# Kernel optimization log

Measured on AMD Instinct MI355X. Metric: run time of the kernel, lower is better.

Reference implementation:

```python
import jax, jax.numpy as jnp
import numpy as np

EPS = 1e-5

def _ln(x, g, b):
    mu = jnp.mean(x, axis=-1, keepdims=True)
    var = jnp.mean((x - mu) ** 2, axis=-1, keepdims=True)
    return (x - mu) * jax.lax.rsqrt(var + EPS) * g + b

def setup_inputs() -> dict:
    key = jax.random.key(0)
    B, V, I, H = 32, 48, 24, 768
    ks = jax.random.split(key, 10)
    s = 0.02
    return {
        'variables': jax.random.normal(ks[0], (B, V, H), jnp.float32),
        'interventions': jax.random.normal(ks[1], (B, I, H), jnp.float32),
        # variable_encoder: Linear(H,H) + LayerNorm(H)
        'W_enc': jax.random.normal(ks[2], (H, H), jnp.float32) * s,
        'b_enc': jnp.zeros((H,), jnp.float32),
        'g_enc': jnp.ones((H,), jnp.float32),
        'be_enc': jnp.zeros((H,), jnp.float32),
        # graph_generator: Linear(2H,H) + LN(H) + ReLU + Linear(H,1) + Sigmoid
        'Wg1': jax.random.normal(ks[3], (2 * H, H), jnp.float32) * s,
        'bg1': jnp.zeros((H,), jnp.float32),
        'g_g': jnp.ones((H,), jnp.float32),
        'b_g': jnp.zeros((H,), jnp.float32),
        'Wg2': jax.random.normal(ks[4], (H, 1), jnp.float32) * s,
        'bg2': jnp.zeros((1,), jnp.float32),
        # intervention_predictor: Linear(2H,H) + LN(H) + ReLU + Linear(H,H)
        'Wi1': jax.random.normal(ks[5], (2 * H, H), jnp.float32) * s,
        'bi1': jnp.zeros((H,), jnp.float32),
        'g_i': jnp.ones((H,), jnp.float32),
        'b_i': jnp.zeros((H,), jnp.float32),
        'Wi2': jax.random.normal(ks[6], (H, H), jnp.float32) * s,
        'bi2': jnp.zeros((H,), jnp.float32),
    }

def reference(variables, interventions, W_enc, b_enc, g_enc, be_enc,
              Wg1, bg1, g_g, b_g, Wg2, bg2, Wi1, bi1, g_i, b_i, Wi2, bi2):
    H = variables.shape[-1]
    V = variables.shape[1]
    # variable encoder: Linear + LayerNorm + ReLU
    enc = jax.nn.relu(_ln(variables @ W_enc + b_enc, g_enc, be_enc))  # [B,V,H]

    # graph generator over all ordered pairs (i,j): concat([enc_i, enc_j]) @ Wg1
    # split Wg1 so the concat-matmul becomes two small GEMMs + broadcast add
    hi = jnp.einsum('bvh,hk->bvk', enc, Wg1[:H])   # contribution of enc_i
    hj = jnp.einsum('bvh,hk->bvk', enc, Wg1[H:])   # contribution of enc_j
    h = jax.nn.relu(_ln(hi[:, :, None, :] + hj[:, None, :, :] + bg1, g_g, b_g))  # [B,V,V,H]
    score = jax.nn.sigmoid(jnp.squeeze(h @ Wg2, -1) + bg2[0])  # [B,V,V]
    # diagonal (i==j) is never written in the original -> stays zero
    causal_graph = score * (1.0 - jnp.eye(V, dtype=score.dtype))

    # intervention predictor: concat([intervention_i, enc_j]) -> MLP
    ha = jnp.einsum('bih,hk->bik', interventions, Wi1[:H])  # [B,I,H]
    hb = jnp.einsum('bvh,hk->bvk', enc, Wi1[H:])            # [B,V,H]
    h2 = jax.nn.relu(_ln(ha[:, :, None, :] + hb[:, None, :, :] + bi1, g_i, b_i))  # [B,I,V,H]
    effects = h2 @ Wi2 + bi2  # [B,I,V,H]

    return (effects, causal_graph, enc)
```

## Files before the change

kernel.cpp:

```cpp
#include <hip/hip_runtime.h>
#include <math.h>

#define Bp 32
#define Vp 48
#define Ip 24
#define Hp 768
#define EPS 1e-5f

#define EFFECTS_SIZE (Bp*Ip*Vp*Hp)
#define GRAPH_SIZE   (Bp*Vp*Vp)
#define ENC_SIZE     (Bp*Vp*Hp)
#define MS           (Hp*Hp)

typedef __attribute__((ext_vector_type(8))) short short8;
typedef __attribute__((ext_vector_type(4))) float floatx4;
typedef __attribute__((ext_vector_type(4))) unsigned int uintx4;

__device__ __forceinline__ unsigned short f2bf(float f) {
    unsigned int u = __float_as_uint(f);
    u += 0x7fffu + ((u >> 16) & 1u);
    return (unsigned short)(u >> 16);
}
__device__ __forceinline__ unsigned int f2bf2(float a, float b) {
    return (unsigned int)f2bf(a) | ((unsigned int)f2bf(b) << 16);
}

__global__ __launch_bounds__(256) void pack_weights(
    const float* __restrict__ W_enc, const float* __restrict__ Wg1,
    const float* __restrict__ Wi1, const float* __restrict__ Wi2,
    unsigned short* __restrict__ packed)
{
    const int bid = blockIdx.x;
    const int m = bid / 288;
    const int rem = bid - m * 288;
    const int T = rem / 6;
    const int u = rem - T * 6;
    const float* src;
    switch (m) {
        case 0: src = W_enc; break;
        case 1: src = Wg1; break;
        case 2: src = Wg1 + Hp * Hp; break;
        case 3: src = Wi1 + Hp * Hp; break;
        case 4: src = Wi1; break;
        default: src = Wi2; break;
    }
    unsigned short* dst = packed + (size_t)m * MS;
    const int lane = threadIdx.x & 63;
    const int kq = threadIdx.x >> 6;
    const int col = T * 16 + (lane & 15);
    const int krow0 = (lane >> 4) * 8;
    const int kb = kq + 4 * u;
    unsigned int w[4];
#pragma unroll
    for (int p2 = 0; p2 < 4; ++p2) {
        float f0 = src[(size_t)(kb * 32 + krow0 + 2 * p2)     * Hp + col];
        float f1 = src[(size_t)(kb * 32 + krow0 + 2 * p2 + 1) * Hp + col];
        w[p2] = f2bf2(f0, f1);
    }
    uintx4 v; v.x = w[0]; v.y = w[1]; v.z = w[2]; v.w = w[3];
    *(uintx4*)(dst + ((size_t)(T * 24 + kb) * 64 + lane) * 8) = v;
}

__global__ __launch_bounds__(256) void convert_inputs(
    const float* __restrict__ vars, const float* __restrict__ intv,
    const float* __restrict__ bg1, const float* __restrict__ bi1,
    unsigned short* __restrict__ varb, unsigned short* __restrict__ intvb,
    float* __restrict__ bias2304)
{
    const int p = blockIdx.x * 256 + threadIdx.x;
    const int VPn = ENC_SIZE / 2;
    if (p < VPn) {
        float2 f = ((const float2*)vars)[p];
        ((unsigned int*)varb)[p] = f2bf2(f.x, f.y);
    } else {
        int q = p - VPn;
        float2 f = ((const float2*)intv)[q];
        ((unsigned int*)intvb)[q] = f2bf2(f.x, f.y);
    }
    if (blockIdx.x == 0) {
        for (int t = threadIdx.x; t < 2304; t += 256)
            bias2304[t] = (t < 768) ? 0.0f : (t < 1536 ? bg1[t - 768] : bi1[t - 1536]);
    }
}

__global__ __launch_bounds__(256) void gemm48(
    const unsigned short* __restrict__ A, const unsigned short* __restrict__ Bpk,
    const float* __restrict__ bias, float* __restrict__ C, int ldc)
{
    __shared__ unsigned short Asl[3 * 24 * 64 * 8];
    const int tid = threadIdx.x, wave = tid >> 6, lane = tid & 63;
    const int m0 = blockIdx.x * 48;

#pragma unroll
    for (int uu = 0; uu < 18; ++uu) {
        const int s = tid + 256 * uu;
        const int mt = s / 1536;
        const int r2 = s - mt * 1536;
        const int kb = r2 >> 6;
        const int L  = r2 & 63;
        const int mrow = L & 15, kq = L >> 4;
        uintx4 v = *(const uintx4*)(A + (size_t)(m0 + mt * 16 + mrow) * Hp + kb * 32 + kq * 8);
        const int phys = (mt * 24 + kb) * 64 + (L ^ (kb & 7));
        *(uintx4*)(&Asl[phys * 8]) = v;
    }
    __syncthreads();

    const int mrow = lane & 15, kq = lane >> 4;
    const floatx4 z = {0.f, 0.f, 0.f, 0.f};

#pragma unroll
    for (int G = 0; G < 2; ++G) {
        const int Tg0 = blockIdx.y * 48 + wave * 12 + G * 6;
        const unsigned short* Bbase = Bpk + (size_t)Tg0 * 12288 + lane * 8;
        floatx4 acc[3][6];
#pragma unroll
        for (int mt = 0; mt < 3; ++mt)
#pragma unroll
            for (int nt = 0; nt < 6; ++nt) acc[mt][nt] = z;

        short8 bbuf[3][6], abuf[2][3];
#pragma unroll
        for (int nt = 0; nt < 6; ++nt) {
            bbuf[0][nt] = *(const short8*)(Bbase + (size_t)nt * 12288);
            bbuf[1][nt] = *(const short8*)(Bbase + (size_t)nt * 12288 + 512);
        }
#pragma unroll
        for (int mt = 0; mt < 3; ++mt)
            abuf[0][mt] = *(const short8*)(&Asl[((mt * 24) * 64 + lane) * 8]);

#pragma unroll
        for (int kb = 0; kb < 24; ++kb) {
            if (kb + 2 < 24) {
#pragma unroll
                for (int nt = 0; nt < 6; ++nt)
                    bbuf[(kb + 2) % 3][nt] =
                        *(const short8*)(Bbase + (size_t)nt * 12288 + (kb + 2) * 512);
            }
            if (kb + 1 < 24) {
#pragma unroll
                for (int mt = 0; mt < 3; ++mt)
                    abuf[(kb + 1) & 1][mt] = *(const short8*)(
                        &Asl[((mt * 24 + kb + 1) * 64 + (lane ^ ((kb + 1) & 7))) * 8]);
            }
#pragma unroll
            for (int mt = 0; mt < 3; ++mt)
#pragma unroll
                for (int nt = 0; nt < 6; ++nt)
                    acc[mt][nt] = __builtin_amdgcn_mfma_f32_16x16x32_bf16(
                        abuf[kb & 1][mt], bbuf[kb % 3][nt], acc[mt][nt], 0, 0, 0);
        }

#pragma unroll
        for (int nt = 0; nt < 6; ++nt) {
            const int colg = (Tg0 + nt) * 16 + mrow;
            const float bv = bias ? bias[colg] : 0.0f;
#pragma unroll
            for (int mt = 0; mt < 3; ++mt)
#pragma unroll
                for (int r = 0; r < 4; ++r)
                    C[(size_t)(m0 + mt * 16 + kq * 4 + r) * ldc + colg] = acc[mt][nt][r] + bv;
        }
    }
}

__global__ __launch_bounds__(256) void ln_relu(
    const float* __restrict__ pre, const float* __restrict__ g,
    const float* __restrict__ be, float* __restrict__ encf,
    unsigned short* __restrict__ encb)
{
    const int wave = threadIdx.x >> 6, lane = threadIdx.x & 63;
    const int row = blockIdx.x * 4 + wave;
    const float2* rp = (const float2*)(pre + (size_t)row * Hp);
    float2 x[6]; float s = 0.f, q = 0.f;
#pragma unroll
    for (int c = 0; c < 6; ++c) {
        x[c] = rp[lane + 64 * c];
        s += x[c].x + x[c].y;
        q += x[c].x * x[c].x + x[c].y * x[c].y;
    }
#pragma unroll
    for (int m = 1; m < 64; m <<= 1) { s += __shfl_xor(s, m, 64); q += __shfl_xor(q, m, 64); }
    const float mu = s * (1.0f / Hp);
    const float var = q * (1.0f / Hp) - mu * mu;
    const float rs = rsqrtf(var + EPS);
    float2* of = (float2*)(encf + (size_t)row * Hp);
    unsigned int* ob = (unsigned int*)(encb + (size_t)row * Hp);
#pragma unroll
    for (int c = 0; c < 6; ++c) {
        const float2 g2 = ((const float2*)g)[lane + 64 * c];
        const float2 b2 = ((const float2*)be)[lane + 64 * c];
        float y0 = fmaxf((x[c].x - mu) * rs * g2.x + b2.x, 0.f);
        float y1 = fmaxf((x[c].y - mu) * rs * g2.y + b2.y, 0.f);
        of[lane + 64 * c] = make_float2(y0, y1);
        ob[lane + 64 * c] = f2bf2(y0, y1);
    }
}

__global__ __launch_bounds__(256) void graph_kernel(
    const float* __restrict__ ws2, const float* __restrict__ gg_,
    const float* __restrict__ bb_, const float* __restrict__ Wg2,
    const float* __restrict__ bg2, float* __restrict__ out)
{
    const int wave = threadIdx.x >> 6, lane = threadIdx.x & 63;
    const int p = blockIdx.x;
    const int b = p / Vp, i = p - b * Vp;
    const float* hi_row = ws2 + (size_t)p * 2304;
    float ri[12], gg[12], bb[12], w2[12];
#pragma unroll
    for (int c = 0; c < 12; ++c) {
        const int k = lane + 64 * c;
        ri[c] = hi_row[k]; gg[c] = gg_[k]; bb[c] = bb_[k]; w2[c] = Wg2[k];
    }
    const float bg2v = bg2[0];
    const int j0 = wave * 12;
    for (int jj = 0; jj < 12; ++jj) {
        const int j = j0 + jj;
        const float* hj_row = ws2 + (size_t)(b * Vp + j) * 2304 + 768;
        float x[12], s = 0.f, q = 0.f;
#pragma unroll
        for (int c = 0; c < 12; ++c) {
            x[c] = ri[c] + hj_row[lane + 64 * c];
            s += x[c]; q += x[c] * x[c];
        }
#pragma unroll
        for (int m = 1; m < 64; m <<= 1) { s += __shfl_xor(s, m, 64); q += __shfl_xor(q, m, 64); }
        const float mu = s * (1.0f / Hp);
        const float var = q * (1.0f / Hp) - mu * mu;
        const float rs = rsqrtf(var + EPS);
        float pd = 0.f;
#pragma unroll
        for (int c = 0; c < 12; ++c) {
            float y = fmaxf((x[c] - mu) * rs * gg[c] + bb[c], 0.f);
            pd = fmaf(y, w2[c], pd);
        }
#pragma unroll
        for (int m = 1; m < 64; m <<= 1) pd += __shfl_xor(pd, m, 64);
        if (lane == 0) {
            float sc = (i == j) ? 0.0f : 1.0f / (1.0f + expf(-(pd + bg2v)));
            out[(size_t)p * Vp + j] = sc;
        }
    }
}

__global__ __launch_bounds__(256) void effects48(
    const float* __restrict__ ha, const float* __restrict__ ws2,
    const float* __restrict__ g_i, const float* __restrict__ b_i,
    const unsigned short* __restrict__ Bpk, const float* __restrict__ bi2,
    float* __restrict__ out)
{
    __shared__ unsigned short Asl[3 * 24 * 64 * 8];
    const int tid = threadIdx.x, wave = tid >> 6, lane = tid & 63;
    const int bi = blockIdx.x;
    const int b = bi / Ip;
    const int half = lane >> 5, hl = lane & 31;

    const floatx4* hap = (const floatx4*)(ha + (size_t)bi * Hp);
    const floatx4* gp = (const floatx4*)g_i;
    const floatx4* bp = (const floatx4*)b_i;
    floatx4 hav[6], gv[6], bv[6];
#pragma unroll
    for (int t = 0; t < 3; ++t) {
        hav[2*t]   = hap[2*hl + 64*t];     hav[2*t+1] = hap[2*hl + 1 + 64*t];
        gv[2*t]    = gp[2*hl + 64*t];      gv[2*t+1]  = gp[2*hl + 1 + 64*t];
        bv[2*t]    = bp[2*hl + 64*t];      bv[2*t+1]  = bp[2*hl + 1 + 64*t];
    }

#pragma unroll
    for (int p = 0; p < 6; ++p) {
        const int u = wave * 12 + 2 * p + half;
        const floatx4* hbp = (const floatx4*)(ws2 + (size_t)(b * Vp + u) * 2304 + 1536);
        floatx4 x[6]; float s = 0.f, q = 0.f;
#pragma unroll
        for (int t = 0; t < 3; ++t) {
            x[2*t]   = hav[2*t]   + hbp[2*hl + 64*t];
            x[2*t+1] = hav[2*t+1] + hbp[2*hl + 1 + 64*t];
        }
#pragma unroll
        for (int c = 0; c < 6; ++c) {
            s += x[c].x + x[c].y + x[c].z + x[c].w;
            q += x[c].x*x[c].x + x[c].y*x[c].y + x[c].z*x[c].z + x[c].w*x[c].w;
        }
#pragma unroll
        for (int m = 1; m < 32; m <<= 1) { s += __shfl_xor(s, m, 64); q += __shfl_xor(q, m, 64); }
        const float mu = s * (1.0f / Hp);
        const float var = q * (1.0f / Hp) - mu * mu;
        const float rs = rsqrtf(var + EPS);
        const int mt = u >> 4, mrow = u & 15;
#pragma unroll
        for (int t = 0; t < 3; ++t) {
            float y0 = fmaxf((x[2*t].x   - mu) * rs * gv[2*t].x   + bv[2*t].x,   0.f);
            float y1 = fmaxf((x[2*t].y   - mu) * rs * gv[2*t].y   + bv[2*t].y,   0.f);
            float y2 = fmaxf((x[2*t].z   - mu) * rs * gv[2*t].z   + bv[2*t].z,   0.f);
            float y3 = fmaxf((x[2*t].w   - mu) * rs * gv[2*t].w   + bv[2*t].w,   0.f);
            float y4 = fmaxf((x[2*t+1].x - mu) * rs * gv[2*t+1].x + bv[2*t+1].x, 0.f);
            float y5 = fmaxf((x[2*t+1].y - mu) * rs * gv[2*t+1].y + bv[2*t+1].y, 0.f);
            float y6 = fmaxf((x[2*t+1].z - mu) * rs * gv[2*t+1].z + bv[2*t+1].z, 0.f);
            float y7 = fmaxf((x[2*t+1].w - mu) * rs * gv[2*t+1].w + bv[2*t+1].w, 0.f);
            const int cpk = hl + 32 * t;
            const int kb = cpk >> 2, kq2 = cpk & 3;
            const int phys = (mt * 24 + kb) * 64 + ((kq2 * 16 + mrow) ^ (kb & 7));
            uintx4 v;
            v.x = f2bf2(y0, y1); v.y = f2bf2(y2, y3);
            v.z = f2bf2(y4, y5); v.w = f2bf2(y6, y7);
            *(uintx4*)(&Asl[phys * 8]) = v;
        }
    }
    __syncthreads();

    const int mrow = lane & 15, kq = lane >> 4;
    const floatx4 z = {0.f, 0.f, 0.f, 0.f};
#pragma unroll
    for (int G = 0; G < 2; ++G) {
        const int Tg0 = wave * 12 + G * 6;
        const unsigned short* Bbase = Bpk + (size_t)Tg0 * 12288 + lane * 8;
        floatx4 acc[3][6];
#pragma unroll
        for (int mt = 0; mt < 3; ++mt)
#pragma unroll
            for (int nt = 0; nt < 6; ++nt) acc[mt][nt] = z;

        short8 bbuf[3][6], abuf[2][3];
#pragma unroll
        for (int nt = 0; nt < 6; ++nt) {
            bbuf[0][nt] = *(const short8*)(Bbase + (size_t)nt * 12288);
            bbuf[1][nt] = *(const short8*)(Bbase + (size_t)nt * 12288 + 512);
        }
#pragma unroll
        for (int mt = 0; mt < 3; ++mt)
            abuf[0][mt] = *(const short8*)(&Asl[((mt * 24) * 64 + lane) * 8]);

#pragma unroll
        for (int kb = 0; kb < 24; ++kb) {
            if (kb + 2 < 24) {
#pragma unroll
                for (int nt = 0; nt < 6; ++nt)
                    bbuf[(kb + 2) % 3][nt] =
                        *(const short8*)(Bbase + (size_t)nt * 12288 + (kb + 2) * 512);
            }
            if (kb + 1 < 24) {
#pragma unroll
                for (int mt = 0; mt < 3; ++mt)
                    abuf[(kb + 1) & 1][mt] = *(const short8*)(
                        &Asl[((mt * 24 + kb + 1) * 64 + (lane ^ ((kb + 1) & 7))) * 8]);
            }
#pragma unroll
            for (int mt = 0; mt < 3; ++mt)
#pragma unroll
                for (int nt = 0; nt < 6; ++nt)
                    acc[mt][nt] = __builtin_amdgcn_mfma_f32_16x16x32_bf16(
                        abuf[kb & 1][mt], bbuf[kb % 3][nt], acc[mt][nt], 0, 0, 0);
        }

#pragma unroll
        for (int nt = 0; nt < 6; ++nt) {
            const int colg = (Tg0 + nt) * 16 + mrow;
            const float biasv = bi2[colg];
#pragma unroll
            for (int mt = 0; mt < 3; ++mt) {
#pragma unroll
                for (int r = 0; r < 4; ++r) {
                    out[(size_t)(bi * 48 + mt * 16 + kq * 4 + r) * Hp + colg] =
                        acc[mt][nt][r] + biasv;
                }
            }
        }
    }
}

extern "C" void kernel_launch(void* const* d_in, const int* in_sizes, int n_in,
                              void* d_out, int out_size, void* d_ws, size_t ws_size,
                              hipStream_t stream) {
    const float* variables     = (const float*)d_in[0];
    const float* interventions = (const float*)d_in[1];
    const float* W_enc  = (const float*)d_in[2];
    const float* b_enc  = (const float*)d_in[3];
    const float* g_enc  = (const float*)d_in[4];
    const float* be_enc = (const float*)d_in[5];
    const float* Wg1 = (const float*)d_in[6];
    const float* bg1 = (const float*)d_in[7];
    const float* g_g = (const float*)d_in[8];
    const float* b_g = (const float*)d_in[9];
    const float* Wg2 = (const float*)d_in[10];
    const float* bg2 = (const float*)d_in[11];
    const float* Wi1 = (const float*)d_in[12];
    const float* bi1 = (const float*)d_in[13];
    const float* g_i = (const float*)d_in[14];
    const float* b_i = (const float*)d_in[15];
    const float* Wi2 = (const float*)d_in[16];
    const float* bi2 = (const float*)d_in[17];

    float* out = (float*)d_out;
    float* effects = out;
    float* graph = out + EFFECTS_SIZE;
    float* enc_f = out + EFFECTS_SIZE + GRAPH_SIZE;

    char* wsb = (char*)d_ws;
    unsigned short* packedW = (unsigned short*)wsb;
    float* ws2  = (float*)(wsb + 7077888);
    float* pre1 = ws2;
    float* ha   = (float*)(wsb + 7077888 + 14155776);
    unsigned short* varb  = (unsigned short*)(wsb + 23592960);
    unsigned short* intvb = (unsigned short*)(wsb + 25952256);
    unsigned short* encb  = (unsigned short*)(wsb + 27131904);
    float* bias2304 = (float*)(wsb + 29491200);

    pack_weights<<<1728, 256, 0, stream>>>(W_enc, Wg1, Wi1, Wi2, packedW);
    convert_inputs<<<3456, 256, 0, stream>>>(variables, interventions, bg1, bi1,
                                             varb, intvb, bias2304);
    gemm48<<<dim3(32, 1), 256, 0, stream>>>(varb, packedW, b_enc, pre1, Hp);
    ln_relu<<<384, 256, 0, stream>>>(pre1, g_enc, be_enc, enc_f, encb);
    gemm48<<<dim3(32, 3), 256, 0, stream>>>(encb, packedW + (size_t)1 * MS,
                                            bias2304, ws2, 2304);
    gemm48<<<dim3(16, 1), 256, 0, stream>>>(intvb, packedW + (size_t)4 * MS,
                                            nullptr, ha, Hp);
    graph_kernel<<<Bp * Vp, 256, 0, stream>>>(ws2, g_g, b_g, Wg2, bg2, graph);
    effects48<<<Bp * Ip, 256, 0, stream>>>(ha, ws2, g_i, b_i,
                                           packedW + (size_t)5 * MS, bi2, effects);
}
```

Measured before the change: 335.8 us.

## Shrink GEMM tiles for more blocks and stagger K/wave order to spread weight reads

Replaces the 48-row GEMM with a 32-row, 48-column-per-block variant launched on a much larger grid, so the small projection GEMMs fill more compute units instead of 32 or 96 blocks. Both the small GEMMs and the effects kernel now rotate their K-loop starting chunk and permute wave-to-column assignment per block, so concurrent blocks read different parts of the packed weights at the same time. The B prefetch depth grows from 2 to 3 stages. In exchange each block reuses weights less and more A tiles are loaded redundantly, and register use rises from the deeper buffer.

```diff
diff --git a/kernel.cpp b/kernel.cpp
--- a/kernel.cpp
+++ b/kernel.cpp
@@ -83,83 +83,88 @@
     }
 }
 
-__global__ __launch_bounds__(256) void gemm48(
+__global__ __launch_bounds__(256) void gemm32(
     const unsigned short* __restrict__ A, const unsigned short* __restrict__ Bpk,
     const float* __restrict__ bias, float* __restrict__ C, int ldc)
 {
-    __shared__ unsigned short Asl[3 * 24 * 64 * 8];
+    __shared__ unsigned short Asl[2 * 24 * 64 * 8];
     const int tid = threadIdx.x, wave = tid >> 6, lane = tid & 63;
-    const int m0 = blockIdx.x * 48;
-
-#pragma unroll
-    for (int uu = 0; uu < 18; ++uu) {
+    const int m0 = blockIdx.x * 32;
+
+#pragma unroll
+    for (int uu = 0; uu < 12; ++uu) {
         const int s = tid + 256 * uu;
         const int mt = s / 1536;
         const int r2 = s - mt * 1536;
         const int kb = r2 >> 6;
         const int L  = r2 & 63;
-        const int mrow = L & 15, kq = L >> 4;
-        uintx4 v = *(const uintx4*)(A + (size_t)(m0 + mt * 16 + mrow) * Hp + kb * 32 + kq * 8);
-        const int phys = (mt * 24 + kb) * 64 + (L ^ (kb & 7));
-        *(uintx4*)(&Asl[phys * 8]) = v;
+        uintx4 v = *(const uintx4*)(A + (size_t)(m0 + mt * 16 + (L & 15)) * Hp
+                                      + kb * 32 + (L >> 4) * 8);
+        *(uintx4*)(&Asl[((mt * 24 + kb) * 64 + (L ^ (kb & 7))) * 8]) = v;
     }
     __syncthreads();
 
     const int mrow = lane & 15, kq = lane >> 4;
+    const int rot = ((blockIdx.x * 5 + blockIdx.y) & 7) * 3;
+    const int wavep = (wave + blockIdx.x) & 3;
+    const int Tg0 = blockIdx.y * 12 + wavep * 3;
+    const unsigned short* Bbase = Bpk + (size_t)Tg0 * 12288 + lane * 8;
+
     const floatx4 z = {0.f, 0.f, 0.f, 0.f};
-
-#pragma unroll
-    for (int G = 0; G < 2; ++G) {
-        const int Tg0 = blockIdx.y * 48 + wave * 12 + G * 6;
-        const unsigned short* Bbase = Bpk + (size_t)Tg0 * 12288 + lane * 8;
-        floatx4 acc[3][6];
-#pragma unroll
-        for (int mt = 0; mt < 3; ++mt)
-#pragma unroll
-            for (int nt = 0; nt < 6; ++nt) acc[mt][nt] = z;
-
-        short8 bbuf[3][6], abuf[2][3];
-#pragma unroll
-        for (int nt = 0; nt < 6; ++nt) {
-            bbuf[0][nt] = *(const short8*)(Bbase + (size_t)nt * 12288);
-            bbuf[1][nt] = *(const short8*)(Bbase + (size_t)nt * 12288 + 512);
-        }
-#pragma unroll
-        for (int mt = 0; mt < 3; ++mt)
-            abuf[0][mt] = *(const short8*)(&Asl[((mt * 24) * 64 + lane) * 8]);
-
-#pragma unroll
-        for (int kb = 0; kb < 24; ++kb) {
-            if (kb + 2 < 24) {
-#pragma unroll
-                for (int nt = 0; nt < 6; ++nt)
-                    bbuf[(kb + 2) % 3][nt] =
-                        *(const short8*)(Bbase + (size_t)nt * 12288 + (kb + 2) * 512);
-            }
-            if (kb + 1 < 24) {
-#pragma unroll
-                for (int mt = 0; mt < 3; ++mt)
-                    abuf[(kb + 1) & 1][mt] = *(const short8*)(
-                        &Asl[((mt * 24 + kb + 1) * 64 + (lane ^ ((kb + 1) & 7))) * 8]);
-            }
-#pragma unroll
-            for (int mt = 0; mt < 3; ++mt)
-#pragma unroll
-                for (int nt = 0; nt < 6; ++nt)
-                    acc[mt][nt] = __builtin_amdgcn_mfma_f32_16x16x32_bf16(
-                        abuf[kb & 1][mt], bbuf[kb % 3][nt], acc[mt][nt], 0, 0, 0);
-        }
-
-#pragma unroll
-        for (int nt = 0; nt < 6; ++nt) {
-            const int colg = (Tg0 + nt) * 16 + mrow;
-            const float bv = bias ? bias[colg] : 0.0f;
-#pragma unroll
-            for (int mt = 0; mt < 3; ++mt)
-#pragma unroll
-                for (int r = 0; r < 4; ++r)
-                    C[(size_t)(m0 + mt * 16 + kq * 4 + r) * ldc + colg] = acc[mt][nt][r] + bv;
-        }
+    floatx4 acc[2][3];
+#pragma unroll
+    for (int mt = 0; mt < 2; ++mt)
+#pragma unroll
+        for (int nt = 0; nt < 3; ++nt) acc[mt][nt] = z;
+
+    short8 bbuf[4][3], abuf[2][2];
+#pragma unroll
+    for (int d = 0; d < 3; ++d) {
+        int kc = d + rot; if (kc >= 24) kc -= 24;
+#pragma unroll
+        for (int nt = 0; nt < 3; ++nt)
+            bbuf[d][nt] = *(const short8*)(Bbase + (size_t)nt * 12288 + kc * 512);
+    }
+    {
+        int kc = rot;
+#pragma unroll
+        for (int mt = 0; mt < 2; ++mt)
+            abuf[0][mt] = *(const short8*)(&Asl[((mt * 24 + kc) * 64 + (lane ^ (kc & 7))) * 8]);
+    }
+
+#pragma unroll
+    for (int kb = 0; kb < 24; ++kb) {
+        if (kb + 3 < 24) {
+            int kc = kb + 3 + rot; if (kc >= 24) kc -= 24;
+#pragma unroll
+            for (int nt = 0; nt < 3; ++nt)
+                bbuf[(kb + 3) & 3][nt] =
+                    *(const short8*)(Bbase + (size_t)nt * 12288 + kc * 512);
+        }
+        if (kb + 1 < 24) {
+            int kc = kb + 1 + rot; if (kc >= 24) kc -= 24;
+#pragma unroll
+            for (int mt = 0; mt < 2; ++mt)
+                abuf[(kb + 1) & 1][mt] = *(const short8*)(
+                    &Asl[((mt * 24 + kc) * 64 + (lane ^ (kc & 7))) * 8]);
+        }
+#pragma unroll
+        for (int mt = 0; mt < 2; ++mt)
+#pragma unroll
+            for (int nt = 0; nt < 3; ++nt)
+                acc[mt][nt] = __builtin_amdgcn_mfma_f32_16x16x32_bf16(
+                    abuf[kb & 1][mt], bbuf[kb & 3][nt], acc[mt][nt], 0, 0, 0);
+    }
+
+#pragma unroll
+    for (int nt = 0; nt < 3; ++nt) {
+        const int colg = (Tg0 + nt) * 16 + mrow;
+        const float bv = bias ? bias[colg] : 0.0f;
+#pragma unroll
+        for (int mt = 0; mt < 2; ++mt)
+#pragma unroll
+            for (int r = 0; r < 4; ++r)
+                C[(size_t)(m0 + mt * 16 + kq * 4 + r) * ldc + colg] = acc[mt][nt][r] + bv;
     }
 }
 
@@ -308,10 +313,12 @@
     __syncthreads();
 
     const int mrow = lane & 15, kq = lane >> 4;
+    const int rot = (bi & 7) * 3;
+    const int wavep = (wave + bi) & 3;
     const floatx4 z = {0.f, 0.f, 0.f, 0.f};
 #pragma unroll
     for (int G = 0; G < 2; ++G) {
-        const int Tg0 = wave * 12 + G * 6;
+        const int Tg0 = wavep * 12 + G * 6;
         const unsigned short* Bbase = Bpk + (size_t)Tg0 * 12288 + lane * 8;
         floatx4 acc[3][6];
 #pragma unroll
@@ -319,36 +326,43 @@
 #pragma unroll
             for (int nt = 0; nt < 6; ++nt) acc[mt][nt] = z;
 
-        short8 bbuf[3][6], abuf[2][3];
-#pragma unroll
-        for (int nt = 0; nt < 6; ++nt) {
-            bbuf[0][nt] = *(const short8*)(Bbase + (size_t)nt * 12288);
-            bbuf[1][nt] = *(const short8*)(Bbase + (size_t)nt * 12288 + 512);
-        }
-#pragma unroll
-        for (int mt = 0; mt < 3; ++mt)
-            abuf[0][mt] = *(const short8*)(&Asl[((mt * 24) * 64 + lane) * 8]);
+        short8 bbuf[4][6], abuf[2][3];
+#pragma unroll
+        for (int d = 0; d < 3; ++d) {
+            int kc = d + rot; if (kc >= 24) kc -= 24;
+#pragma unroll
+            for (int nt = 0; nt < 6; ++nt)
+                bbuf[d][nt] = *(const short8*)(Bbase + (size_t)nt * 12288 + kc * 512);
+        }
+        {
+            int kc = rot;
+#pragma unroll
+            for (int mt = 0; mt < 3; ++mt)
+                abuf[0][mt] = *(const short8*)(&Asl[((mt * 24 + kc) * 64 + (lane ^ (kc & 7))) * 8]);
+        }
 
 #pragma unroll
         for (int kb = 0; kb < 24; ++kb) {
-            if (kb + 2 < 24) {
+            if (kb + 3 < 24) {
+                int kc = kb + 3 + rot; if (kc >= 24) kc -= 24;
 #pragma unroll
                 for (int nt = 0; nt < 6; ++nt)
-                    bbuf[(kb + 2) % 3][nt] =
-                        *(const short8*)(Bbase + (size_t)nt * 12288 + (kb + 2) * 512);
+                    bbuf[(kb + 3) & 3][nt] =
+                        *(const short8*)(Bbase + (size_t)nt * 12288 + kc * 512);
             }
             if (kb + 1 < 24) {
+                int kc = kb + 1 + rot; if (kc >= 24) kc -= 24;
 #pragma unroll
                 for (int mt = 0; mt < 3; ++mt)
                     abuf[(kb + 1) & 1][mt] = *(const short8*)(
-                        &Asl[((mt * 24 + kb + 1) * 64 + (lane ^ ((kb + 1) & 7))) * 8]);
+                        &Asl[((mt * 24 + kc) * 64 + (lane ^ (kc & 7))) * 8]);
             }
 #pragma unroll
             for (int mt = 0; mt < 3; ++mt)
 #pragma unroll
                 for (int nt = 0; nt < 6; ++nt)
                     acc[mt][nt] = __builtin_amdgcn_mfma_f32_16x16x32_bf16(
-                        abuf[kb & 1][mt], bbuf[kb % 3][nt], acc[mt][nt], 0, 0, 0);
+                        abuf[kb & 1][mt], bbuf[kb & 3][nt], acc[mt][nt], 0, 0, 0);
         }
 
 #pragma unroll
@@ -407,11 +421,11 @@
     pack_weights<<<1728, 256, 0, stream>>>(W_enc, Wg1, Wi1, Wi2, packedW);
     convert_inputs<<<3456, 256, 0, stream>>>(variables, interventions, bg1, bi1,
                                              varb, intvb, bias2304);
-    gemm48<<<dim3(32, 1), 256, 0, stream>>>(varb, packedW, b_enc, pre1, Hp);
+    gemm32<<<dim3(48, 4), 256, 0, stream>>>(varb, packedW, b_enc, pre1, Hp);
     ln_relu<<<384, 256, 0, stream>>>(pre1, g_enc, be_enc, enc_f, encb);
-    gemm48<<<dim3(32, 3), 256, 0, stream>>>(encb, packedW + (size_t)1 * MS,
-                                            bias2304, ws2, 2304);
-    gemm48<<<dim3(16, 1), 256, 0, stream>>>(intvb, packedW + (size_t)4 * MS,
+    gemm32<<<dim3(48, 12), 256, 0, stream>>>(encb, packedW + (size_t)1 * MS,
+                                             bias2304, ws2, 2304);
+    gemm32<<<dim3(24, 4), 256, 0, stream>>>(intvb, packedW + (size_t)4 * MS,
                                             nullptr, ha, Hp);
     graph_kernel<<<Bp * Vp, 256, 0, stream>>>(ws2, g_g, b_g, Wg2, bg2, graph);
     effects48<<<Bp * Ip, 256, 0, stream>>>(ha, ws2, g_i, b_i,
```

Measured after the change: 312.1 us. 1.08x faster.
